# Performance work log

Hardware: AMD Instinct MI355X
Metric: run time of the kernel (lower is better)

The kernel has to match this reference:

```python
import jax, jax.numpy as jnp
import numpy as np
from jax import lax

PI = 3.141592653
TWO_PI = 2.0 * PI
IOU_THR = 0.3


def limit_period(val):
    return val - jnp.floor(val / TWO_PI + 0.5) * TWO_PI


def box_corners_bev(b):
    # b: [7] = (x, y, z, dx, dy, dz, heading) -> [4,2] CCW BEV corners
    signs = jnp.array([[0.5, -0.5], [0.5, 0.5], [-0.5, 0.5], [-0.5, -0.5]], jnp.float32)
    local = signs * jnp.stack([b[3], b[4]])
    c, s = jnp.cos(b[6]), jnp.sin(b[6])
    rot_t = jnp.stack([jnp.stack([c, s]), jnp.stack([-s, c])])  # R^T
    return local @ rot_t + jnp.stack([b[0], b[1]])


def clip_halfplane(poly, cnt, a, b):
    # Sutherland-Hodgman: clip poly[:cnt] (CCW) by left side of edge a->b. Buffer V=8.
    V = poly.shape[0]
    idx = jnp.arange(V)
    nxt = jnp.where(idx + 1 < cnt, idx + 1, 0)
    p1, p2 = poly, poly[nxt]
    e = b - a
    d1 = e[0] * (p1[:, 1] - a[1]) - e[1] * (p1[:, 0] - a[0])
    d2 = e[0] * (p2[:, 1] - a[1]) - e[1] * (p2[:, 0] - a[0])
    in1, in2 = d1 >= 0, d2 >= 0
    valid = idx < cnt
    denom = d1 - d2
    t = d1 / jnp.where(jnp.abs(denom) > 1e-8, denom, 1.0)
    inter = p1 + t[:, None] * (p2 - p1)
    emit = jnp.stack([in1 & valid, (in1 ^ in2) & valid], 1).reshape(2 * V)
    vals = jnp.stack([p1, inter], 1).reshape(2 * V, 2)
    pos = jnp.cumsum(emit) - 1
    scatter_idx = jnp.where(emit, pos, 2 * V)  # out-of-range -> dropped
    new_poly = jnp.zeros((V, 2), poly.dtype).at[scatter_idx].set(vals, mode='drop')
    return new_poly, emit.sum().astype(jnp.int32)


def poly_area(poly, cnt):
    V = poly.shape[0]
    idx = jnp.arange(V)
    nxt = jnp.where(idx + 1 < cnt, idx + 1, 0)
    p2 = poly[nxt]
    cr = poly[:, 0] * p2[:, 1] - p2[:, 0] * poly[:, 1]
    return 0.5 * jnp.abs(jnp.sum(jnp.where(idx < cnt, cr, 0.0)))


def pair_iou3d(ba, bb):
    pa, pb = box_corners_bev(ba), box_corners_bev(bb)
    poly = jnp.zeros((8, 2), jnp.float32).at[:4].set(pa)
    cnt = jnp.int32(4)
    for k in range(4):
        poly, cnt = clip_halfplane(poly, cnt, pb[k], pb[(k + 1) % 4])
    inter_bev = poly_area(poly, cnt)
    top = jnp.minimum(ba[2] + 0.5 * ba[5], bb[2] + 0.5 * bb[5])
    bot = jnp.maximum(ba[2] - 0.5 * ba[5], bb[2] - 0.5 * bb[5])
    inter = inter_bev * jnp.maximum(top - bot, 0.0)
    va = ba[3] * ba[4] * ba[5]
    vb = bb[3] * bb[4] * bb[5]
    return inter / jnp.maximum(va + vb - inter, 1e-6)


def pairwise_iou3d(boxes):
    return jax.vmap(lambda a: jax.vmap(lambda b: pair_iou3d(a, b))(boxes))(boxes)


def clustering(ious):
    # Faithful port of the sequential while-loop: repeatedly take first unassigned
    # box and stamp everything with iou > 0.3 to the current cluster id.
    n = ious.shape[0]

    def body(i, carry):
        ci, cur = carry
        unassigned = ci == 0
        has = jnp.any(unassigned)
        first = jnp.argmax(unassigned)
        m = ious[first] > IOU_THR
        ci = jnp.where(has & m, cur, ci)
        return ci, cur + jnp.where(has, 1, 0).astype(jnp.int32)

    ci, _ = lax.fori_loop(0, n, body, (jnp.zeros(n, jnp.int32), jnp.int32(1)))
    return ci


def cluster_fusion(boxes, scores, cluster_indices):
    # Masked, vmapped version of per-cluster weighted circular-mean fusion.
    # Output row (cid-1) is the fused box for cluster cid; empty slots are zero.
    n = boxes.shape[0]

    def fuse_one(cid):
        mask = cluster_indices == cid
        valid = jnp.any(mask)
        s = jnp.where(mask, scores, 0.0)
        dirs = boxes[:, 6]
        d0 = dirs[jnp.argmax(jnp.where(mask, scores, -jnp.inf))]
        diff = jnp.abs(dirs - d0)
        diff = jnp.where(diff > PI, TWO_PI - diff, diff)
        gt = diff > PI / 2
        flip_gt = jnp.sum(s * gt) <= jnp.sum(s * (~gt))
        dirs = jnp.where(jnp.where(flip_gt, gt, ~gt), dirs + PI, dirs)
        dirs = limit_period(dirs)
        sn = s / jnp.where(valid, jnp.sum(s), 1.0)
        sint = jnp.where(valid, jnp.sum(jnp.sin(dirs) * sn), 0.0)
        cost = jnp.where(valid, jnp.sum(jnp.cos(dirs) * sn), 1.0)
        theta = jnp.arctan2(sint, cost)
        center_dim = jnp.sum(boxes[:, :6] * sn[:, None], axis=0)
        return jnp.where(valid, jnp.concatenate([center_dim, theta[None]]), 0.0)

    return jax.vmap(fuse_one)(jnp.arange(1, n + 1, dtype=jnp.int32))


def setup_inputs() -> dict:
    key = jax.random.key(0)
    k1, k2, k3, k4, k5, k6 = jax.random.split(key, 6)
    N, G = 1024, 256  # 1024 detections clustered around 256 locations
    anchors = jax.random.uniform(k1, (G, 2), minval=-60.0, maxval=60.0)
    xy = anchors[jnp.repeat(jnp.arange(G), N // G)] + 0.8 * jax.random.normal(k2, (N, 2))
    z = jax.random.uniform(k3, (N, 1), minval=-1.0, maxval=1.0)
    dims = jax.random.uniform(k4, (N, 3), minval=jnp.array([3.5, 1.5, 1.4]),
                              maxval=jnp.array([4.5, 2.0, 1.8]))
    heading = jax.random.uniform(k5, (N, 1), minval=-PI, maxval=PI)
    pred_boxes = jnp.concatenate([xy, z, dims, heading], axis=1).astype(jnp.float32)
    pred_scores = jax.random.uniform(k6, (N,), minval=0.1, maxval=1.0)
    return {"pred_boxes": pred_boxes, "pred_scores": pred_scores}


def reference(pred_boxes, pred_scores):
    boxes = pred_boxes.at[:, 6].set(limit_period(pred_boxes[:, 6]))
    ious = pairwise_iou3d(boxes)
    ci = clustering(ious)
    return cluster_fusion(boxes, pred_scores, ci)
```

## Files before the change

### kernel.cpp

```cpp
#include <hip/hip_runtime.h>
#include <math.h>

#define NBOX 1024
#define PI_F 3.141592653f
#define TWO_PI_F 6.283185306f
#define HALF_PI_F 1.5707963265f
#define IOU_THR_F 0.3f

__device__ __forceinline__ float limit_period_f(float v) {
    return v - floorf(v / TWO_PI_F + 0.5f) * TWO_PI_F;
}

__device__ __forceinline__ void clip_edge(float (&px)[8], float (&py)[8], int &cnt,
                                          float axp, float ayp, float bxp, float byp) {
    float ex = bxp - axp, ey = byp - ayp;
    float d[8];
#pragma unroll
    for (int v = 0; v < 8; ++v)
        d[v] = ex * (py[v] - ayp) - ey * (px[v] - axp);

    float cxv[16], cyv[16];
    bool fl[16];
#pragma unroll
    for (int v = 0; v < 8; ++v) {
        bool valid = v < cnt;
        bool wrap = !(v + 1 < cnt);
        float p2x = wrap ? px[0] : px[(v + 1) & 7];
        float p2y = wrap ? py[0] : py[(v + 1) & 7];
        float d2v = wrap ? d[0] : d[(v + 1) & 7];
        float d1v = d[v];
        bool in1 = d1v >= 0.0f, in2 = d2v >= 0.0f;
        fl[2 * v] = in1 && valid;
        cxv[2 * v] = px[v];
        cyv[2 * v] = py[v];
        fl[2 * v + 1] = (in1 != in2) && valid;
        float den = d1v - d2v;
        float t = d1v / (fabsf(den) > 1e-8f ? den : 1.0f);
        cxv[2 * v + 1] = px[v] + t * (p2x - px[v]);
        cyv[2 * v + 1] = py[v] + t * (p2y - py[v]);
    }

    int pos = 0;
    float ox[8], oy[8];
#pragma unroll
    for (int o = 0; o < 8; ++o) { ox[o] = 0.0f; oy[o] = 0.0f; }
#pragma unroll
    for (int c = 0; c < 16; ++c) {
#pragma unroll
        for (int o = 0; o < 8; ++o) {
            if (o > c) continue;
            if (fl[c] && pos == o) { ox[o] = cxv[c]; oy[o] = cyv[c]; }
        }
        pos += fl[c] ? 1 : 0;
    }
    cnt = pos > 8 ? 8 : pos;
#pragma unroll
    for (int v = 0; v < 8; ++v) { px[v] = ox[v]; py[v] = oy[v]; }
}

__global__ __launch_bounds__(256) void iou_adj_kernel(const float* __restrict__ boxes,
                                                      unsigned long long* __restrict__ adj) {
    int t = blockIdx.x * 256 + threadIdx.x;
    int i = t >> 10;
    int j = t & 1023;
    const float* ba = boxes + i * 7;
    const float* bb = boxes + j * 7;
    float ax = ba[0], ay = ba[1], az = ba[2], al = ba[3], aw = ba[4], ah = ba[5];
    float bx = bb[0], by = bb[1], bz = bb[2], bl = bb[3], bw = bb[4], bh = bb[5];
    float tha = limit_period_f(ba[6]);
    float thb = limit_period_f(bb[6]);

    bool hit = false;
    float dx = ax - bx, dy = ay - by;
    float ra = 0.5f * sqrtf(al * al + aw * aw);
    float rb = 0.5f * sqrtf(bl * bl + bw * bw);
    float top = fminf(az + 0.5f * ah, bz + 0.5f * bh);
    float bot = fmaxf(az - 0.5f * ah, bz - 0.5f * bh);
    float hov = fmaxf(top - bot, 0.0f);
    float rr = ra + rb;
    if (dx * dx + dy * dy <= rr * rr && hov > 0.0f) {
        float ca = cosf(tha), sa = sinf(tha);
        float cb = cosf(thb), sb = sinf(thb);

        float px[8], py[8];
        {
            float hx = 0.5f * al, hy = 0.5f * aw;
            float sxv[4] = { hx, hx, -hx, -hx };
            float syv[4] = { -hy, hy, hy, -hy };
#pragma unroll
            for (int k = 0; k < 4; ++k) {
                px[k] = sxv[k] * ca - syv[k] * sa + ax;
                py[k] = sxv[k] * sa + syv[k] * ca + ay;
            }
#pragma unroll
            for (int k = 4; k < 8; ++k) { px[k] = 0.0f; py[k] = 0.0f; }
        }
        float qx[4], qy[4];
        {
            float hx = 0.5f * bl, hy = 0.5f * bw;
            float sxv[4] = { hx, hx, -hx, -hx };
            float syv[4] = { -hy, hy, hy, -hy };
#pragma unroll
            for (int k = 0; k < 4; ++k) {
                qx[k] = sxv[k] * cb - syv[k] * sb + bx;
                qy[k] = sxv[k] * sb + syv[k] * cb + by;
            }
        }
        int cnt = 4;
#pragma unroll
        for (int k = 0; k < 4; ++k)
            clip_edge(px, py, cnt, qx[k], qy[k], qx[(k + 1) & 3], qy[(k + 1) & 3]);

        float s2 = 0.0f;
#pragma unroll
        for (int v = 0; v < 8; ++v) {
            bool valid = v < cnt;
            bool wrap = !(v + 1 < cnt);
            float p2x = wrap ? px[0] : px[(v + 1) & 7];
            float p2y = wrap ? py[0] : py[(v + 1) & 7];
            float cr = px[v] * p2y - p2x * py[v];
            s2 += valid ? cr : 0.0f;
        }
        float area = 0.5f * fabsf(s2);
        float inter = area * hov;
        float va = al * aw * ah, vb = bl * bw * bh;
        float iou = inter / fmaxf(va + vb - inter, 1e-6f);
        hit = iou > IOU_THR_F;
    }
    unsigned long long bal = __ballot(hit);
    if ((threadIdx.x & 63) == 0)
        adj[t >> 6] = bal;
}

__global__ __launch_bounds__(1024) void cluster_kernel(const unsigned long long* __restrict__ adj,
                                                       int* __restrict__ ci,
                                                       int* __restrict__ nclust_out) {
    __shared__ unsigned long long sA[NBOX * 16];
    __shared__ int sseq[NBOX];
    __shared__ int part[16][64];
    const unsigned short* sA16 = (const unsigned short*)sA;
    int tid = threadIdx.x;
#pragma unroll
    for (int j = 0; j < 16; ++j)
        sA[j * 1024 + tid] = adj[j * 1024 + tid];
    __syncthreads();

    int wid = tid >> 6;
    int lane = tid & 63;

    if (wid == 0) {
        unsigned int um = 0xFFFFu;
        int cur = 1;
        for (int t = 0; t < 16; ++t) {
            unsigned long long dv = sA[(t * 64 + lane) * 16 + t];
            unsigned int dlo = (unsigned int)dv;
            unsigned int dhi = (unsigned int)(dv >> 32);
            unsigned long long c =
                ((unsigned long long)((unsigned int)__builtin_amdgcn_readlane((int)um, 4 * t)     & 0xFFFFu)) |
                ((unsigned long long)((unsigned int)__builtin_amdgcn_readlane((int)um, 4 * t + 1) & 0xFFFFu) << 16) |
                ((unsigned long long)((unsigned int)__builtin_amdgcn_readlane((int)um, 4 * t + 2) & 0xFFFFu) << 32) |
                ((unsigned long long)((unsigned int)__builtin_amdgcn_readlane((int)um, 4 * t + 3) & 0xFFFFu) << 48);
            unsigned long long M = 0ull;
            unsigned int kill = 0u;
            while (c) {
                int s = __ffsll((long long)c) - 1;
                unsigned long long Ws =
                    ((unsigned long long)(unsigned int)__builtin_amdgcn_readlane((int)dhi, s) << 32) |
                    (unsigned long long)(unsigned int)__builtin_amdgcn_readlane((int)dlo, s);
                M |= (1ull << s);
                c &= ~Ws;
                c &= ~(1ull << s);
                kill |= (unsigned int)sA16[(t * 64 + s) * 64 + lane];
            }
            um &= ~kill;
            unsigned int mlo = (unsigned int)M, mhi = (unsigned int)(M >> 32);
            int rank = __builtin_amdgcn_mbcnt_hi(mhi, __builtin_amdgcn_mbcnt_lo(mlo, 0));
            int sd = (int)((M >> lane) & 1ull);
            sseq[t * 64 + lane] = sd ? (cur + rank) : 0;
            cur += __builtin_popcountll(M);
        }
        if (lane == 0)
            *nclust_out = cur - 1;
    }
    __syncthreads();

    int cg[16];
#pragma unroll
    for (int g = 0; g < 16; ++g) cg[g] = 0;
    int rbase = wid * 64;
#pragma unroll 4
    for (int d = 0; d < 64; ++d) {
        int r = rbase + d;
        unsigned int x = sA16[r * 64 + lane];
        int sq = sseq[r];
#pragma unroll
        for (int g = 0; g < 16; ++g) {
            bool h = ((x >> g) & 1u) != 0u;
            cg[g] = (h && sq > cg[g]) ? sq : cg[g];
        }
    }
#pragma unroll
    for (int g = 0; g < 16; ++g) {
        part[wid][lane] = cg[g];
        __syncthreads();
        if (wid == 0) {
            int m = part[0][lane];
#pragma unroll
            for (int w = 1; w < 16; ++w) m = m > part[w][lane] ? m : part[w][lane];
            ci[lane * 16 + g] = m;
        }
        __syncthreads();
    }
}

__global__ __launch_bounds__(256) void fusion_kernel(const float* __restrict__ boxes,
                                                     const float* __restrict__ scores,
                                                     const int* __restrict__ ci,
                                                     const int* __restrict__ nclust_p,
                                                     float* __restrict__ out) {
    __shared__ float sb[NBOX][7];
    __shared__ float ss[NBOX];
    __shared__ int   sc[NBOX];
    int tid = threadIdx.x;
    int nclust = *nclust_p;

    if (blockIdx.x * 4 + 1 > nclust) {
        if (tid < 28) {
            out[blockIdx.x * 28 + tid] = 0.0f;
        }
        return;
    }

    for (int idx = tid; idx < NBOX * 7; idx += 256) {
        float v = boxes[idx];
        int col = idx % 7;
        if (col == 6) v = limit_period_f(v);
        sb[idx / 7][col] = v;
    }
    for (int b = tid; b < NBOX; b += 256) {
        ss[b] = scores[b];
        sc[b] = ci[b];
    }
    __syncthreads();

    int wave = tid >> 6;
    int lane = tid & 63;
    int cid = blockIdx.x * 4 + wave + 1;

    float bv = -INFINITY;
    int bi = 0;
    for (int c = 0; c < 16; ++c) {
        int b = c * 64 + lane;
        float v = (sc[b] == cid) ? ss[b] : -INFINITY;
        if (v > bv) { bv = v; bi = b; }
    }
#pragma unroll
    for (int off = 32; off > 0; off >>= 1) {
        float ov = __shfl_xor(bv, off);
        int   oi = __shfl_xor(bi, off);
        if (ov > bv || (ov == bv && oi < bi)) { bv = ov; bi = oi; }
    }
    float* o = out + (cid - 1) * 7;
    if (!(bv > -INFINITY)) {
        if (lane == 0) {
#pragma unroll
            for (int jj = 0; jj < 7; ++jj) o[jj] = 0.0f;
        }
        return;
    }
    float d0 = sb[bi][6];

    float sgt = 0.0f, sngt = 0.0f, ssum = 0.0f;
    for (int c = 0; c < 16; ++c) {
        int b = c * 64 + lane;
        float s = (sc[b] == cid) ? ss[b] : 0.0f;
        float diff = fabsf(sb[b][6] - d0);
        diff = (diff > PI_F) ? (TWO_PI_F - diff) : diff;
        bool gt = diff > HALF_PI_F;
        sgt += gt ? s : 0.0f;
        sngt += gt ? 0.0f : s;
        ssum += s;
    }
#pragma unroll
    for (int off = 32; off > 0; off >>= 1) {
        sgt  += __shfl_xor(sgt, off);
        sngt += __shfl_xor(sngt, off);
        ssum += __shfl_xor(ssum, off);
    }
    bool flip = (sgt <= sngt);
    float inv = ssum;

    float sint = 0.0f, cost = 0.0f;
    float acc[6] = { 0.0f, 0.0f, 0.0f, 0.0f, 0.0f, 0.0f };
    for (int c = 0; c < 16; ++c) {
        int b = c * 64 + lane;
        float s = (sc[b] == cid) ? ss[b] : 0.0f;
        float sn = s / inv;
        float dH = sb[b][6];
        float diff = fabsf(dH - d0);
        diff = (diff > PI_F) ? (TWO_PI_F - diff) : diff;
        bool gt = diff > HALF_PI_F;
        bool cond = flip ? gt : !gt;
        float dd = cond ? (dH + PI_F) : dH;
        dd = limit_period_f(dd);
        sint += sinf(dd) * sn;
        cost += cosf(dd) * sn;
#pragma unroll
        for (int jj = 0; jj < 6; ++jj)
            acc[jj] += sb[b][jj] * sn;
    }
#pragma unroll
    for (int off = 32; off > 0; off >>= 1) {
        sint += __shfl_xor(sint, off);
        cost += __shfl_xor(cost, off);
#pragma unroll
        for (int jj = 0; jj < 6; ++jj)
            acc[jj] += __shfl_xor(acc[jj], off);
    }

    if (lane == 0) {
#pragma unroll
        for (int jj = 0; jj < 6; ++jj) o[jj] = acc[jj];
        o[6] = atan2f(sint, cost);
    }
}

extern "C" void kernel_launch(void* const* d_in, const int* in_sizes, int n_in,
                              void* d_out, int out_size, void* d_ws, size_t ws_size,
                              hipStream_t stream) {
    const float* boxes  = (const float*)d_in[0];
    const float* scores = (const float*)d_in[1];
    unsigned long long* adj = (unsigned long long*)d_ws;
    int* ci     = (int*)d_ws;
    int* nclust = (int*)((char*)d_ws + 4096);
    float* out = (float*)d_out;

    iou_adj_kernel<<<(NBOX * NBOX) / 256, 256, 0, stream>>>(boxes, adj);
    cluster_kernel<<<1, 1024, 0, stream>>>(adj, ci, nclust);
    fusion_kernel<<<NBOX / 4, 256, 0, stream>>>(boxes, scores, ci, nclust, out);
}
```

Before: 181.2 us.

## Unroll greedy cluster scan branch-free and reduce cluster ids via shared atomics

The serial greedy clustering loop over each 64-box tile becomes a fully unrolled, branch-free sweep over all 64 candidates. The tile's adjacency columns are preloaded into registers, so the scan no longer has a data-dependent while loop with dependent LDS loads. The final per-column max reduction swaps 16 rounds of shared-memory write, barrier and serial reduce for LDS atomicMax into a shared array followed by one barrier. The trade-off is always doing all 64 iterations per tile and higher register pressure from the 64-entry preload.

Result: faster. 160.8 us (-11.3%).

```diff
diff --git a/kernel.cpp b/kernel.cpp
--- a/kernel.cpp
+++ b/kernel.cpp
@@ -137,12 +137,13 @@
                                                        int* __restrict__ nclust_out) {
     __shared__ unsigned long long sA[NBOX * 16];
     __shared__ int sseq[NBOX];
-    __shared__ int part[16][64];
+    __shared__ int cimax[NBOX];
     const unsigned short* sA16 = (const unsigned short*)sA;
     int tid = threadIdx.x;
 #pragma unroll
     for (int j = 0; j < 16; ++j)
         sA[j * 1024 + tid] = adj[j * 1024 + tid];
+    cimax[tid] = 0;
     __syncthreads();
 
     int wid = tid >> 6;
@@ -155,6 +156,10 @@
             unsigned long long dv = sA[(t * 64 + lane) * 16 + t];
             unsigned int dlo = (unsigned int)dv;
             unsigned int dhi = (unsigned int)(dv >> 32);
+            unsigned short tb[64];
+#pragma unroll
+            for (int k = 0; k < 64; ++k)
+                tb[k] = sA16[(t * 64 + k) * 64 + lane];
             unsigned long long c =
                 ((unsigned long long)((unsigned int)__builtin_amdgcn_readlane((int)um, 4 * t)     & 0xFFFFu)) |
                 ((unsigned long long)((unsigned int)__builtin_amdgcn_readlane((int)um, 4 * t + 1) & 0xFFFFu) << 16) |
@@ -162,21 +167,22 @@
                 ((unsigned long long)((unsigned int)__builtin_amdgcn_readlane((int)um, 4 * t + 3) & 0xFFFFu) << 48);
             unsigned long long M = 0ull;
             unsigned int kill = 0u;
-            while (c) {
-                int s = __ffsll((long long)c) - 1;
-                unsigned long long Ws =
-                    ((unsigned long long)(unsigned int)__builtin_amdgcn_readlane((int)dhi, s) << 32) |
-                    (unsigned long long)(unsigned int)__builtin_amdgcn_readlane((int)dlo, s);
-                M |= (1ull << s);
-                c &= ~Ws;
-                c &= ~(1ull << s);
-                kill |= (unsigned int)sA16[(t * 64 + s) * 64 + lane];
+#pragma unroll
+            for (int k = 0; k < 64; ++k) {
+                unsigned int wl = (unsigned int)__builtin_amdgcn_readlane((int)dlo, k);
+                unsigned int wh = (unsigned int)__builtin_amdgcn_readlane((int)dhi, k);
+                unsigned long long W = ((unsigned long long)wh << 32) | (unsigned long long)wl;
+                unsigned long long sd = (c >> k) & 1ull;
+                unsigned long long msk = 0ull - sd;
+                M |= msk & (1ull << k);
+                c &= ~(msk & W);
+                kill |= ((unsigned int)(0u - (unsigned int)sd)) & (unsigned int)tb[k];
             }
             um &= ~kill;
             unsigned int mlo = (unsigned int)M, mhi = (unsigned int)(M >> 32);
             int rank = __builtin_amdgcn_mbcnt_hi(mhi, __builtin_amdgcn_mbcnt_lo(mlo, 0));
-            int sd = (int)((M >> lane) & 1ull);
-            sseq[t * 64 + lane] = sd ? (cur + rank) : 0;
+            int sd2 = (int)((M >> lane) & 1ull);
+            sseq[t * 64 + lane] = sd2 ? (cur + rank) : 0;
             cur += __builtin_popcountll(M);
         }
         if (lane == 0)
@@ -200,17 +206,10 @@
         }
     }
 #pragma unroll
-    for (int g = 0; g < 16; ++g) {
-        part[wid][lane] = cg[g];
-        __syncthreads();
-        if (wid == 0) {
-            int m = part[0][lane];
-#pragma unroll
-            for (int w = 1; w < 16; ++w) m = m > part[w][lane] ? m : part[w][lane];
-            ci[lane * 16 + g] = m;
-        }
-        __syncthreads();
-    }
+    for (int g = 0; g < 16; ++g)
+        atomicMax(&cimax[lane * 16 + g], cg[g]);
+    __syncthreads();
+    ci[tid] = cimax[tid];
 }
 
 __global__ __launch_bounds__(256) void fusion_kernel(const float* __restrict__ boxes,
```
